# Performance work log

Hardware: AMD Instinct MI355X
Metric: run time of the kernel (lower is better)

## Reference

```python
import jax, jax.numpy as jnp
import numpy as np
from jax import lax

SEG = 256          # total_length == seg_length
SMOOTH_K = 9       # odd smoothing kernel
BASE_AMP = 0.08


def effective_pattern(pattern_i, pattern_q):
    # [2, SEG]
    p = jnp.stack([pattern_i, pattern_q], axis=0)
    # avg_pool1d(kernel=K, stride=1, pad=K//2, count_include_pad=True)
    # == 'same' convolution with a uniform kernel and zero padding
    ker = jnp.ones((SMOOTH_K,), p.dtype) / SMOOTH_K
    p = jax.vmap(lambda row: jnp.convolve(row, ker, mode='same'))(p)
    p = p - p.mean(axis=1, keepdims=True)            # per-channel demean
    rms = jnp.sqrt(jnp.mean(p * p) + 1e-8)           # global RMS
    return p / rms * BASE_AMP                        # [2, SEG]


def setup_inputs() -> dict:
    key = jax.random.key(0)
    k1, k2, k3, k4 = jax.random.split(key, 4)
    B, L = 4096, 4096
    x = jax.random.normal(k1, (B, 2, L), dtype=jnp.float32)
    pattern_i = jax.random.normal(k2, (SEG,), dtype=jnp.float32)
    pattern_q = jax.random.normal(k3, (SEG,), dtype=jnp.float32)
    starts = jax.random.randint(k4, (B,), 0, L - SEG + 1, dtype=jnp.int32)
    return {"x": x, "pattern_i": pattern_i, "pattern_q": pattern_q, "starts": starts}


def reference(x, pattern_i, pattern_q, starts):
    pat = effective_pattern(pattern_i, pattern_q)            # [2, SEG]
    # adaptive amplitude: per-sample signal RMS over (channel, time)
    amp = jnp.sqrt(jnp.mean(x * x, axis=(1, 2), keepdims=True) + 1e-12)  # [B,1,1]
    upd = amp * pat[None, :, :]                               # [B, 2, SEG]

    def add_one(xb, ub, s):
        # xb: [2, L], ub: [2, SEG], s: scalar start (always in-range)
        seg = lax.dynamic_slice(xb, (0, s), (2, SEG))
        return lax.dynamic_update_slice(xb, seg + ub, (0, s))

    return jax.vmap(add_one)(x, upd, starts)
```

## Files before the change

kernel.cpp:

```cpp
#include <hip/hip_runtime.h>

#define SEG 256
#define SMOOTH_K 9
#define BASE_AMP 0.08f
#define L 4096
#define ROW (2 * L)

__global__ __launch_bounds__(256) void pattern_kernel(
    const float* __restrict__ pi, const float* __restrict__ pq,
    float* __restrict__ pat_out) {
    __shared__ float wsum0[4], wsum1[4], wsq[4];

    const int i = threadIdx.x;
    float v0 = 0.f, v1 = 0.f;
    #pragma unroll
    for (int j = -(SMOOTH_K / 2); j <= SMOOTH_K / 2; ++j) {
        int k = i + j;
        if (k >= 0 && k < SEG) { v0 += pi[k]; v1 += pq[k]; }
    }
    v0 *= (1.0f / SMOOTH_K);
    v1 *= (1.0f / SMOOTH_K);

    float s0 = v0, s1 = v1;
    #pragma unroll
    for (int off = 32; off; off >>= 1) {
        s0 += __shfl_down(s0, off);
        s1 += __shfl_down(s1, off);
    }
    const int wid = i >> 6, lane = i & 63;
    if (lane == 0) { wsum0[wid] = s0; wsum1[wid] = s1; }
    __syncthreads();
    const float m0 = (wsum0[0] + wsum0[1] + wsum0[2] + wsum0[3]) * (1.0f / SEG);
    const float m1 = (wsum1[0] + wsum1[1] + wsum1[2] + wsum1[3]) * (1.0f / SEG);
    const float d0 = v0 - m0;
    const float d1 = v1 - m1;

    float q = d0 * d0 + d1 * d1;
    #pragma unroll
    for (int off = 32; off; off >>= 1) q += __shfl_down(q, off);
    if (lane == 0) wsq[wid] = q;
    __syncthreads();
    const float msq = (wsq[0] + wsq[1] + wsq[2] + wsq[3]) * (1.0f / (2 * SEG));
    const float scale = BASE_AMP / sqrtf(msq + 1e-8f);

    pat_out[i]       = d0 * scale;
    pat_out[SEG + i] = d1 * scale;
}

__global__ __launch_bounds__(256) void apply_kernel(
    const float* __restrict__ x, const int* __restrict__ starts,
    const float* __restrict__ pat, float* __restrict__ out) {
    const int b = blockIdx.x;
    const int t = threadIdx.x;

    const float4* __restrict__ xr =
        reinterpret_cast<const float4*>(x + (size_t)b * ROW);
    float4* __restrict__ outr = reinterpret_cast<float4*>(out + (size_t)b * ROW);

    __shared__ float  spat[2 * SEG];
    __shared__ float4 stash[2 * 66];
    __shared__ float  wred[4];

    spat[t]       = pat[t];
    spat[t + SEG] = pat[t + SEG];

    const int s    = starts[b];
    const int s4   = s >> 2;
    const int e4   = (s + SEG - 1) >> 2;
    const int nper = e4 - s4 + 1;

    float ssq = 0.f;
    #pragma unroll
    for (int k = 0; k < 8; ++k) {
        const int idx = t + k * 256;
        float4 v = xr[idx];
        ssq += v.x * v.x + v.y * v.y + v.z * v.z + v.w * v.w;
        const int c  = idx >> 10;
        const int l4 = idx & 1023;
        if (l4 >= s4 && l4 <= e4) {
            stash[c * 66 + (l4 - s4)] = v;
        } else {
            outr[idx] = v;
        }
    }

    #pragma unroll
    for (int off = 32; off; off >>= 1) ssq += __shfl_down(ssq, off);
    if ((t & 63) == 0) wred[t >> 6] = ssq;
    __syncthreads();
    const float amp =
        sqrtf((wred[0] + wred[1] + wred[2] + wred[3]) * (1.0f / ROW) + 1e-12f);

    if (t < 2 * nper) {
        const int c  = (t >= nper) ? 1 : 0;
        const int j  = t - c * nper;
        const int l4 = s4 + j;
        float4 v = stash[c * 66 + j];
        const float* __restrict__ pc = spat + c * SEG;
        const int r = (l4 << 2) - s;
        if (r >= 0     && r < SEG)     v.x += amp * pc[r];
        if (r + 1 >= 0 && r + 1 < SEG) v.y += amp * pc[r + 1];
        if (r + 2 >= 0 && r + 2 < SEG) v.z += amp * pc[r + 2];
        if (r + 3 >= 0 && r + 3 < SEG) v.w += amp * pc[r + 3];
        outr[(c << 10) + l4] = v;
    }
}

extern "C" void kernel_launch(void* const* d_in, const int* in_sizes, int n_in,
                              void* d_out, int out_size, void* d_ws,
                              size_t ws_size, hipStream_t stream) {
    const float* x      = (const float*)d_in[0];
    const float* pi     = (const float*)d_in[1];
    const float* pq     = (const float*)d_in[2];
    const int*   starts = (const int*)d_in[3];
    float* out = (float*)d_out;
    float* pat = (float*)d_ws;

    const int B = in_sizes[0] / ROW;

    pattern_kernel<<<1, 256, 0, stream>>>(pi, pq, pat);
    apply_kernel<<<B, 256, 0, stream>>>(x, starts, pat, out);
}
```

Before: 242.2 us.

## Split apply into grid-stride copy-reduce kernel plus separate patch kernel

Replaces the one-block-per-row fused kernel with a grid-stride kernel that copies all of x to out and accumulates each row's sum of squares through per-wavefront atomics. A third kernel then rereads the 256-element window and writes it with the pattern added. The pattern is stored zero-padded so the bounds checks become clamped indices. The aim is a better-streaming bulk copy, at the cost of an extra launch, atomics, and rewriting the window region a second time.

Measured after the change: 270.2 us. +11.5%, slower.

```diff
diff --git a/kernel.cpp b/kernel.cpp
--- a/kernel.cpp
+++ b/kernel.cpp
@@ -5,13 +5,19 @@
 #define BASE_AMP 0.08f
 #define L 4096
 #define ROW (2 * L)
+#define ROW4 (ROW / 4)
+
+#define WS_SSQ 768
 
 __global__ __launch_bounds__(256) void pattern_kernel(
     const float* __restrict__ pi, const float* __restrict__ pq,
-    float* __restrict__ pat_out) {
+    float* __restrict__ ws, int B) {
     __shared__ float wsum0[4], wsum1[4], wsq[4];
 
     const int i = threadIdx.x;
+
+    for (int k = i; k < B; k += 256) ws[WS_SSQ + k] = 0.f;
+
     float v0 = 0.f, v1 = 0.f;
     #pragma unroll
     for (int j = -(SMOOTH_K / 2); j <= SMOOTH_K / 2; ++j) {
@@ -43,67 +49,57 @@
     const float msq = (wsq[0] + wsq[1] + wsq[2] + wsq[3]) * (1.0f / (2 * SEG));
     const float scale = BASE_AMP / sqrtf(msq + 1e-8f);
 
-    pat_out[i]       = d0 * scale;
-    pat_out[SEG + i] = d1 * scale;
+    ws[1 + i]       = d0 * scale;
+    ws[258 + 1 + i] = d1 * scale;
+    if (i == 0) { ws[0] = 0.f; ws[257] = 0.f; ws[258] = 0.f; ws[515] = 0.f; }
 }
 
-__global__ __launch_bounds__(256) void apply_kernel(
+__global__ __launch_bounds__(256) void copy_reduce_kernel(
+    const float4* __restrict__ x4, float4* __restrict__ out4,
+    float* __restrict__ ssq, int n4) {
+    int i = blockIdx.x * 256 + threadIdx.x;
+    const int stride = gridDim.x * 256;
+    for (; i < n4; i += stride) {
+        const float4 v = x4[i];
+        out4[i] = v;
+        float q = v.x * v.x + v.y * v.y + v.z * v.z + v.w * v.w;
+        #pragma unroll
+        for (int off = 32; off; off >>= 1) q += __shfl_down(q, off);
+        if ((threadIdx.x & 63) == 0) atomicAdd(&ssq[i >> 11], q);
+    }
+}
+
+__global__ __launch_bounds__(192) void patch_kernel(
     const float* __restrict__ x, const int* __restrict__ starts,
-    const float* __restrict__ pat, float* __restrict__ out) {
+    const float* __restrict__ ws, float* __restrict__ out) {
     const int b = blockIdx.x;
     const int t = threadIdx.x;
+
+    const int s    = starts[b];
+    const int s4   = s >> 2;
+    const int e4   = (s + SEG - 1) >> 2;
+    const int nper = e4 - s4 + 1;
+    if (t >= 2 * nper) return;
+
+    const float amp = sqrtf(ws[WS_SSQ + b] * (1.0f / ROW) + 1e-12f);
+
+    const int c  = (t >= nper) ? 1 : 0;
+    const int j  = t - c * nper;
+    const int l4 = s4 + j;
+    const int idx = (c << 10) + l4;
 
     const float4* __restrict__ xr =
         reinterpret_cast<const float4*>(x + (size_t)b * ROW);
     float4* __restrict__ outr = reinterpret_cast<float4*>(out + (size_t)b * ROW);
 
-    __shared__ float  spat[2 * SEG];
-    __shared__ float4 stash[2 * 66];
-    __shared__ float  wred[4];
-
-    spat[t]       = pat[t];
-    spat[t + SEG] = pat[t + SEG];
-
-    const int s    = starts[b];
-    const int s4   = s >> 2;
-    const int e4   = (s + SEG - 1) >> 2;
-    const int nper = e4 - s4 + 1;
-
-    float ssq = 0.f;
-    #pragma unroll
-    for (int k = 0; k < 8; ++k) {
-        const int idx = t + k * 256;
-        float4 v = xr[idx];
-        ssq += v.x * v.x + v.y * v.y + v.z * v.z + v.w * v.w;
-        const int c  = idx >> 10;
-        const int l4 = idx & 1023;
-        if (l4 >= s4 && l4 <= e4) {
-            stash[c * 66 + (l4 - s4)] = v;
-        } else {
-            outr[idx] = v;
-        }
-    }
-
-    #pragma unroll
-    for (int off = 32; off; off >>= 1) ssq += __shfl_down(ssq, off);
-    if ((t & 63) == 0) wred[t >> 6] = ssq;
-    __syncthreads();
-    const float amp =
-        sqrtf((wred[0] + wred[1] + wred[2] + wred[3]) * (1.0f / ROW) + 1e-12f);
-
-    if (t < 2 * nper) {
-        const int c  = (t >= nper) ? 1 : 0;
-        const int j  = t - c * nper;
-        const int l4 = s4 + j;
-        float4 v = stash[c * 66 + j];
-        const float* __restrict__ pc = spat + c * SEG;
-        const int r = (l4 << 2) - s;
-        if (r >= 0     && r < SEG)     v.x += amp * pc[r];
-        if (r + 1 >= 0 && r + 1 < SEG) v.y += amp * pc[r + 1];
-        if (r + 2 >= 0 && r + 2 < SEG) v.z += amp * pc[r + 2];
-        if (r + 3 >= 0 && r + 3 < SEG) v.w += amp * pc[r + 3];
-        outr[(c << 10) + l4] = v;
-    }
+    float4 v = xr[idx];
+    const float* __restrict__ pc = ws + c * 258;
+    const int r = (l4 << 2) - s;
+    v.x += amp * pc[1 + min(max(r,     -1), SEG)];
+    v.y += amp * pc[1 + min(max(r + 1, -1), SEG)];
+    v.z += amp * pc[1 + min(max(r + 2, -1), SEG)];
+    v.w += amp * pc[1 + min(max(r + 3, -1), SEG)];
+    outr[idx] = v;
 }
 
 extern "C" void kernel_launch(void* const* d_in, const int* in_sizes, int n_in,
@@ -114,10 +110,14 @@
     const float* pq     = (const float*)d_in[2];
     const int*   starts = (const int*)d_in[3];
     float* out = (float*)d_out;
-    float* pat = (float*)d_ws;
+    float* ws  = (float*)d_ws;
 
-    const int B = in_sizes[0] / ROW;
+    const int B  = in_sizes[0] / ROW;
+    const int n4 = B * ROW4;
 
-    pattern_kernel<<<1, 256, 0, stream>>>(pi, pq, pat);
-    apply_kernel<<<B, 256, 0, stream>>>(x, starts, pat, out);
+    pattern_kernel<<<1, 256, 0, stream>>>(pi, pq, ws, B);
+    copy_reduce_kernel<<<2048, 256, 0, stream>>>(
+        reinterpret_cast<const float4*>(x), reinterpret_cast<float4*>(out),
+        ws + WS_SSQ, n4);
+    patch_kernel<<<B, 192, 0, stream>>>(x, starts, ws, out);
 }
```
